# Performance work log

Hardware: AMD Instinct MI355X
Metric: run time of the kernel (lower is better)

Reference implementation:

```python
import jax, jax.numpy as jnp
import numpy as np

N_NODES = 50000
N_EDGES = 800000

def _gcn_layer(x, W, b, src, dst, n):
    # DGL GraphConv, norm='both': out = D_in^{-1/2} A D_out^{-1/2} x W + b
    e = src.shape[0]
    ones = jnp.ones((e,), dtype=x.dtype)
    deg_out = jax.ops.segment_sum(ones, src, num_segments=n)
    deg_in = jax.ops.segment_sum(ones, dst, num_segments=n)
    norm_src = jax.lax.rsqrt(jnp.clip(deg_out, 1.0))  # [n]
    norm_dst = jax.lax.rsqrt(jnp.clip(deg_in, 1.0))   # [n]
    # weight applied before aggregation (in_feats >= out_feats path in DGL)
    h = (x * norm_src[:, None]) @ W                   # [n, out]
    agg = jax.ops.segment_sum(h[src], dst, num_segments=n)  # SpMM: gather-scatter
    return agg * norm_dst[:, None] + b

def setup_inputs() -> dict:
    key = jax.random.key(0)
    ks = jax.random.split(key, 7)
    d_in, d_hid, d_out = 512, 256, 128
    features = jax.random.normal(ks[0], (N_NODES, d_in), dtype=jnp.float32)
    src = jax.random.randint(ks[1], (N_EDGES,), 0, N_NODES, dtype=jnp.int64)
    dst = jax.random.randint(ks[2], (N_EDGES,), 0, N_NODES, dtype=jnp.int64)
    W1 = jax.random.normal(ks[3], (d_in, d_hid), dtype=jnp.float32) / np.sqrt(d_in)
    b1 = jnp.zeros((d_hid,), dtype=jnp.float32)
    W2 = jax.random.normal(ks[4], (d_hid, d_out), dtype=jnp.float32) / np.sqrt(d_hid)
    b2 = jnp.zeros((d_out,), dtype=jnp.float32)
    return {"features": features, "src": src, "dst": dst,
            "W1": W1, "b1": b1, "W2": W2, "b2": b2}

def reference(features, src, dst, W1, b1, W2, b2):
    n = features.shape[0]
    x = _gcn_layer(features, W1, b1, src, dst, n)
    x = jax.nn.relu(x)
    x = _gcn_layer(x, W2, b2, src, dst, n)
    return x
```

## Files before the change

### kernel.cpp

```cpp
#include <hip/hip_runtime.h>
#include <type_traits>

#define DIN  512
#define DHID 256
#define DOF  128

#define RB   13
#define RSZ  (1 << RB)
#define BPR  32

typedef _Float16 f16;
typedef _Float16 f16x8 __attribute__((ext_vector_type(8)));
typedef _Float16 f16v4 __attribute__((ext_vector_type(4)));
typedef _Float16 f16v2 __attribute__((ext_vector_type(2)));
typedef float f32x4 __attribute__((ext_vector_type(4)));

__global__ __launch_bounds__(256) void hist_deg(const int* __restrict__ src,
                                                const int* __restrict__ dst, int e,
                                                int* __restrict__ cnt_out,
                                                int* __restrict__ cnt_in) {
    __shared__ int h_out[RSZ], h_in[RSZ];
    const int r = blockIdx.x / BPR, b = blockIdx.x % BPR;
    const int base = r << RB;
    const int tid = threadIdx.x;
    for (int j = tid; j < RSZ; j += 256) { h_out[j] = 0; h_in[j] = 0; }
    __syncthreads();

    const int ce = (((e + BPR - 1) / BPR) + 3) & ~3;
    const int s0 = b * ce, s1 = min(s0 + ce, e);
    for (int i = s0 + tid * 4; i < s1; i += 1024) {
        if (i + 3 < s1) {
            int4 sv = *(const int4*)(src + i);
            int4 dv = *(const int4*)(dst + i);
            int v;
            v = sv.x - base; if ((unsigned)v < RSZ) atomicAdd(&h_out[v], 1);
            v = sv.y - base; if ((unsigned)v < RSZ) atomicAdd(&h_out[v], 1);
            v = sv.z - base; if ((unsigned)v < RSZ) atomicAdd(&h_out[v], 1);
            v = sv.w - base; if ((unsigned)v < RSZ) atomicAdd(&h_out[v], 1);
            v = dv.x - base; if ((unsigned)v < RSZ) atomicAdd(&h_in[v], 1);
            v = dv.y - base; if ((unsigned)v < RSZ) atomicAdd(&h_in[v], 1);
            v = dv.z - base; if ((unsigned)v < RSZ) atomicAdd(&h_in[v], 1);
            v = dv.w - base; if ((unsigned)v < RSZ) atomicAdd(&h_in[v], 1);
        } else {
            for (int q = i; q < s1; ++q) {
                int v = src[q] - base; if ((unsigned)v < RSZ) atomicAdd(&h_out[v], 1);
                v = dst[q] - base;     if ((unsigned)v < RSZ) atomicAdd(&h_in[v], 1);
            }
        }
    }
    __syncthreads();
    int* co = cnt_out + (size_t)(r * BPR + b) * RSZ;
    int* ci = cnt_in  + (size_t)(r * BPR + b) * RSZ;
    for (int j = tid; j < RSZ; j += 256) { co[j] = h_out[j]; ci[j] = h_in[j]; }
}

__global__ void sum_base(const int* __restrict__ cnt_out, int* __restrict__ cnt_in,
                         int* __restrict__ deg_in,
                         float* __restrict__ norm_src, float* __restrict__ norm_dst, int n) {
    int d = blockIdx.x * blockDim.x + threadIdx.x;
    if (d >= n) return;
    const int r = d >> RB, j = d & (RSZ - 1);
    int* ci = cnt_in + (size_t)(r * BPR) * RSZ + j;
    int s = 0;
#pragma unroll 4
    for (int b = 0; b < BPR; ++b) {
        int c = ci[(size_t)b * RSZ];
        ci[(size_t)b * RSZ] = s;
        s += c;
    }
    deg_in[d] = s;
    norm_dst[d] = rsqrtf(fmaxf((float)s, 1.0f));
    const int* co = cnt_out + (size_t)(r * BPR) * RSZ + j;
    int s2 = 0;
#pragma unroll 4
    for (int b = 0; b < BPR; ++b) s2 += co[(size_t)b * RSZ];
    norm_src[d] = rsqrtf(fmaxf((float)s2, 1.0f));
}

__global__ __launch_bounds__(256) void scan_part(const int* __restrict__ deg,
                                                 int* __restrict__ partial, int n) {
    const int base = blockIdx.x * 1024;
    const int tid = threadIdx.x;
    int v = 0;
#pragma unroll
    for (int j = 0; j < 4; ++j) {
        int i = base + tid * 4 + j;
        if (i < n) v += deg[i];
    }
    for (int o = 1; o < 64; o <<= 1) v += __shfl_xor(v, o);
    __shared__ int wsum[4];
    if ((tid & 63) == 0) wsum[tid >> 6] = v;
    __syncthreads();
    if (tid == 0) partial[blockIdx.x] = wsum[0] + wsum[1] + wsum[2] + wsum[3];
}

__global__ __launch_bounds__(64) void scan_offsets(int* __restrict__ partial, int nb,
                                                   int* __restrict__ rowptr, int n) {
    const int l = threadIdx.x;
    int orig = (l < nb) ? partial[l] : 0;
    int v = orig;
    for (int o = 1; o < 64; o <<= 1) {
        int u = __shfl_up(v, o);
        if (l >= o) v += u;
    }
    if (l < nb) partial[l] = v - orig;
    if (l == nb - 1) rowptr[n] = v;
}

__global__ __launch_bounds__(256) void scan_apply(const int* __restrict__ deg,
                                                  const int* __restrict__ partial,
                                                  int* __restrict__ rowptr, int n) {
    const int base = blockIdx.x * 1024;
    const int tid = threadIdx.x;
    int x[4]; int s = 0;
#pragma unroll
    for (int j = 0; j < 4; ++j) {
        int i = base + tid * 4 + j;
        x[j] = (i < n) ? deg[i] : 0;
        s += x[j];
    }
    const int l = tid & 63, w = tid >> 6;
    int inc = s;
    for (int o = 1; o < 64; o <<= 1) {
        int u = __shfl_up(inc, o);
        if (l >= o) inc += u;
    }
    __shared__ int wsum[4];
    if (l == 63) wsum[w] = inc;
    __syncthreads();
    int wbase = 0;
    for (int q = 0; q < w; ++q) wbase += wsum[q];
    int excl = partial[blockIdx.x] + wbase + (inc - s);
#pragma unroll
    for (int j = 0; j < 4; ++j) {
        int i = base + tid * 4 + j;
        if (i < n) rowptr[i] = excl;
        excl += x[j];
    }
}

__global__ __launch_bounds__(256) void fill_csr2(const int* __restrict__ src,
                                                 const int* __restrict__ dst, int e,
                                                 const int* __restrict__ rowptr,
                                                 const int* __restrict__ base_in,
                                                 int* __restrict__ csr_src) {
    __shared__ int cur[RSZ];
    const int r = blockIdx.x / BPR, b = blockIdx.x % BPR;
    const int base = r << RB;
    const int tid = threadIdx.x;
    for (int j = tid; j < RSZ; j += 256) cur[j] = 0;
    __syncthreads();

    const int* bi = base_in + (size_t)(r * BPR + b) * RSZ;
    const int ce = (((e + BPR - 1) / BPR) + 3) & ~3;
    const int s0 = b * ce, s1 = min(s0 + ce, e);
    for (int i = s0 + tid * 4; i < s1; i += 1024) {
        if (i + 3 < s1) {
            int4 dv = *(const int4*)(dst + i);
            int4 sv = *(const int4*)(src + i);
            int v;
            v = dv.x - base; if ((unsigned)v < RSZ) { int p = atomicAdd(&cur[v], 1); csr_src[rowptr[base + v] + bi[v] + p] = sv.x; }
            v = dv.y - base; if ((unsigned)v < RSZ) { int p = atomicAdd(&cur[v], 1); csr_src[rowptr[base + v] + bi[v] + p] = sv.y; }
            v = dv.z - base; if ((unsigned)v < RSZ) { int p = atomicAdd(&cur[v], 1); csr_src[rowptr[base + v] + bi[v] + p] = sv.z; }
            v = dv.w - base; if ((unsigned)v < RSZ) { int p = atomicAdd(&cur[v], 1); csr_src[rowptr[base + v] + bi[v] + p] = sv.w; }
        } else {
            for (int q = i; q < s1; ++q) {
                int v = dst[q] - base;
                if ((unsigned)v < RSZ) { int p = atomicAdd(&cur[v], 1); csr_src[rowptr[base + v] + bi[v] + p] = src[q]; }
            }
        }
    }
}

__global__ void transpose_w(const float* __restrict__ W1, const float* __restrict__ W2,
                            f16* __restrict__ w1t, f16* __restrict__ w2t) {
    int t = blockIdx.x * blockDim.x + threadIdx.x;
    if (t < DIN * DHID) {
        int k = t / DHID, c = t % DHID;
        w1t[c * DIN + k] = (f16)W1[t];
    } else {
        int u = t - DIN * DHID;
        if (u < DHID * DOF) {
            int k = u / DOF, c = u % DOF;
            w2t[c * DHID + k] = (f16)W2[u];
        }
    }
}

template<int K, int N, bool A_F32>
__global__ __launch_bounds__(256) void mfma_gemm(const void* __restrict__ Aptr,
                                                 const float* __restrict__ norm,
                                                 const f16* __restrict__ Bt,
                                                 f16* __restrict__ H, int M) {
    constexpr int BM = 128, BN = 128, BK = 32;
    constexpr int NT = K / BK;
    __shared__ __align__(16) f16 smem[BM * BN];

    const int rbase = blockIdx.x * BM;
    const int nbj = blockIdx.y * BN;
    const int tid = threadIdx.x;
    const int l = tid & 63, wid = tid >> 6;
    const int wr = wid >> 1, wc = wid & 1;
    const int fr = l & 15, kg = l >> 4;

    int arow[2], achk[2];
    float ascale[2];
#pragma unroll
    for (int j = 0; j < 2; ++j) {
        int u = tid + j * 256;
        arow[j] = u >> 2; achk[j] = u & 3;
        if (A_F32) {
            int grow = rbase + arow[j];
            ascale[j] = (grow < M) ? norm[grow] : 0.0f;
        }
    }

    struct ABregs {
        float4 a0[2], a1[2];
        f16x8  a16[2];
        f16x8  b[2];
    };

    auto gload = [&](int k0) {
        ABregs r;
#pragma unroll
        for (int j = 0; j < 2; ++j) {
            int grow = rbase + arow[j];
            if (A_F32) {
                if (grow < M) {
                    const float* A = (const float*)Aptr + (long)grow * K + k0 + achk[j] * 8;
                    r.a0[j] = *(const float4*)A;
                    r.a1[j] = *(const float4*)(A + 4);
                } else {
                    r.a0[j] = make_float4(0.f, 0.f, 0.f, 0.f);
                    r.a1[j] = make_float4(0.f, 0.f, 0.f, 0.f);
                }
            } else {
                f16x8 v = {};
                if (grow < M)
                    v = *(const f16x8*)((const f16*)Aptr + (long)grow * K + k0 + achk[j] * 8);
                r.a16[j] = v;
            }
            r.b[j] = *(const f16x8*)(Bt + (long)(nbj + arow[j]) * K + k0 + achk[j] * 8);
        }
        return r;
    };

    auto swrite = [&](int buf, const ABregs& r) {
        f16* As = smem + buf * 8192;
        f16* Bs = As + 4096;
#pragma unroll
        for (int j = 0; j < 2; ++j) {
            f16x8 v;
            if (A_F32) {
                float s = ascale[j];
                v[0] = (f16)(r.a0[j].x * s); v[1] = (f16)(r.a0[j].y * s);
                v[2] = (f16)(r.a0[j].z * s); v[3] = (f16)(r.a0[j].w * s);
                v[4] = (f16)(r.a1[j].x * s); v[5] = (f16)(r.a1[j].y * s);
                v[6] = (f16)(r.a1[j].z * s); v[7] = (f16)(r.a1[j].w * s);
            } else {
                v = r.a16[j];
            }
            int ia = (arow[j] * BK + achk[j] * 8) ^ ((arow[j] & 7) << 3);
            *(f16x8*)&As[ia] = v;
            *(f16x8*)&Bs[ia] = r.b[j];
        }
    };

    f32x4 acc[4][4] = {};

    auto compute = [&](int buf) {
        const f16* As = smem + buf * 8192;
        const f16* Bs = As + 4096;
        f16x8 af[4], bf[4];
#pragma unroll
        for (int m = 0; m < 4; ++m) {
            int row = wr * 64 + m * 16 + fr;
            int ia = (row * BK + kg * 8) ^ ((row & 7) << 3);
            af[m] = *(const f16x8*)&As[ia];
        }
#pragma unroll
        for (int nf = 0; nf < 4; ++nf) {
            int c = wc * 64 + nf * 16 + fr;
            int ib = (c * BK + kg * 8) ^ ((c & 7) << 3);
            bf[nf] = *(const f16x8*)&Bs[ib];
        }
#pragma unroll
        for (int m = 0; m < 4; ++m)
#pragma unroll
            for (int nf = 0; nf < 4; ++nf)
                acc[m][nf] = __builtin_amdgcn_mfma_f32_16x16x32_f16(af[m], bf[nf], acc[m][nf], 0, 0, 0);
    };

    ABregs ra = gload(0);
    swrite(0, ra);
    ABregs rb = gload(BK);

#pragma unroll
    for (int kt = 0; kt < NT; kt += 2) {
        __syncthreads();
        if (kt + 2 < NT) ra = gload((kt + 2) * BK);
        compute(0);
        if (kt + 1 < NT) swrite(1, rb);
        if (kt + 1 < NT) {
            __syncthreads();
            if (kt + 3 < NT) rb = gload((kt + 3) * BK);
            compute(1);
            if (kt + 2 < NT) swrite(0, ra);
        }
    }

    __syncthreads();
#pragma unroll
    for (int m = 0; m < 4; ++m)
#pragma unroll
        for (int nf = 0; nf < 4; ++nf)
#pragma unroll
            for (int i = 0; i < 4; ++i) {
                int row = wr * 64 + m * 16 + (l >> 4) * 4 + i;
                int col = wc * 64 + nf * 16 + (l & 15);
                smem[row * BN + col] = (f16)acc[m][nf][i];
            }
    __syncthreads();
#pragma unroll
    for (int j = 0; j < 8; ++j) {
        int u = tid + j * 256;
        int row = u >> 4, cu = u & 15;
        int grow = rbase + row;
        if (grow < M)
            *(f16x8*)(H + (long)grow * N + nbj + cu * 8) =
                *(const f16x8*)&smem[row * BN + cu * 8];
    }
}

template<int F, bool RELU, bool FOLD, bool OUT_F16>
__global__ __launch_bounds__(256) void aggregate_wave(const f16* __restrict__ H,
                                                      const int* __restrict__ rowptr,
                                                      const int* __restrict__ csr_src,
                                                      const float* __restrict__ norm_dst,
                                                      const float* __restrict__ norm_src,
                                                      const float* __restrict__ bias,
                                                      void* __restrict__ outp, int n) {
    constexpr int VPL = F / 64;
    using vec = typename std::conditional<VPL == 4, f16v4, f16v2>::type;

    const int node = blockIdx.x * 4 + (threadIdx.x >> 6);
    if (node >= n) return;
    const int l = threadIdx.x & 63;
    const int c0 = l * VPL;
    const f16* __restrict__ Hc = H + c0;

    int k = rowptr[node];
    const int end = rowptr[node + 1];

    float acc[VPL] = {};
    for (; k + 3 < end; k += 4) {
        int s0 = csr_src[k];
        int s1 = csr_src[k + 1];
        int s2 = csr_src[k + 2];
        int s3 = csr_src[k + 3];
        vec v0 = *(const vec*)(Hc + (long)s0 * F);
        vec v1 = *(const vec*)(Hc + (long)s1 * F);
        vec v2 = *(const vec*)(Hc + (long)s2 * F);
        vec v3 = *(const vec*)(Hc + (long)s3 * F);
#pragma unroll
        for (int q = 0; q < VPL; ++q) acc[q] += (float)v0[q];
#pragma unroll
        for (int q = 0; q < VPL; ++q) acc[q] += (float)v1[q];
#pragma unroll
        for (int q = 0; q < VPL; ++q) acc[q] += (float)v2[q];
#pragma unroll
        for (int q = 0; q < VPL; ++q) acc[q] += (float)v3[q];
    }
    for (; k < end; ++k) {
        vec v = *(const vec*)(Hc + (long)csr_src[k] * F);
#pragma unroll
        for (int q = 0; q < VPL; ++q) acc[q] += (float)v[q];
    }

    const float nd = norm_dst[node];
    const float ns = FOLD ? norm_src[node] : 1.0f;
#pragma unroll
    for (int q = 0; q < VPL; ++q) {
        float v = acc[q] * nd + bias[c0 + q];
        if (RELU) v = fmaxf(v, 0.0f);
        acc[q] = v * ns;
    }

    if (OUT_F16) {
        vec o;
#pragma unroll
        for (int q = 0; q < VPL; ++q) o[q] = (f16)acc[q];
        *(vec*)((f16*)outp + (long)node * F + c0) = o;
    } else {
        float* op = (float*)outp + (long)node * F + c0;
        if (VPL == 2) {
            *(float2*)op = make_float2(acc[0], acc[1]);
        } else {
#pragma unroll
            for (int q = 0; q < VPL; ++q) op[q] = acc[q];
        }
    }
}

extern "C" void kernel_launch(void* const* d_in, const int* in_sizes, int n_in,
                              void* d_out, int out_size, void* d_ws, size_t ws_size,
                              hipStream_t stream) {
    const float* features = (const float*)d_in[0];
    const int*   src      = (const int*)d_in[1];
    const int*   dst      = (const int*)d_in[2];
    const float* W1       = (const float*)d_in[3];
    const float* b1       = (const float*)d_in[4];
    const float* W2       = (const float*)d_in[5];
    const float* b2       = (const float*)d_in[6];
    float* out = (float*)d_out;

    const int n = in_sizes[0] / DIN;
    const int e = in_sizes[1];

    const int ranges = (n + RSZ - 1) >> RB;
    const size_t cntsz = (size_t)ranges * BPR * RSZ;

    char* ws = (char*)d_ws;
    size_t off = 0;
    auto alloc = [&](size_t bytes) { size_t o = off; off += (bytes + 255) & ~(size_t)255; return o; };
    size_t o_degi   = alloc((size_t)n * 4);
    size_t o_nsrc   = alloc((size_t)n * 4);
    size_t o_ndst   = alloc((size_t)n * 4);
    size_t o_rowptr = alloc((size_t)(n + 1) * 4);
    size_t o_part   = alloc((size_t)64 * 4);
    size_t o_csr    = alloc((size_t)e * 4);
    size_t o_cnto   = alloc(cntsz * 4);
    size_t o_cnti   = alloc(cntsz * 4);
    size_t o_w1t    = alloc((size_t)DIN * DHID * 2);
    size_t o_w2t    = alloc((size_t)DHID * DOF * 2);
    size_t o_h1     = alloc((size_t)n * DHID * 2);
    size_t o_x1     = alloc((size_t)n * DHID * 2);
    size_t o_h2     = alloc((size_t)n * DOF * 2);
    (void)ws_size;

    int*   deg_in   = (int*)(ws + o_degi);
    float* norm_src = (float*)(ws + o_nsrc);
    float* norm_dst = (float*)(ws + o_ndst);
    int*   rowptr   = (int*)(ws + o_rowptr);
    int*   partial  = (int*)(ws + o_part);
    int*   csr_src  = (int*)(ws + o_csr);
    int*   cnt_out  = (int*)(ws + o_cnto);
    int*   cnt_in   = (int*)(ws + o_cnti);
    f16*   w1t      = (f16*)(ws + o_w1t);
    f16*   w2t      = (f16*)(ws + o_w2t);
    f16*   h1       = (f16*)(ws + o_h1);
    f16*   x1       = (f16*)(ws + o_x1);
    f16*   h2       = (f16*)(ws + o_h2);

    const int hblocks = ranges * BPR;
    hist_deg<<<hblocks, 256, 0, stream>>>(src, dst, e, cnt_out, cnt_in);
    sum_base<<<(n + 255) / 256, 256, 0, stream>>>(cnt_out, cnt_in, deg_in,
                                                  norm_src, norm_dst, n);
    const int nb = (n + 1023) / 1024;
    scan_part<<<nb, 256, 0, stream>>>(deg_in, partial, n);
    scan_offsets<<<1, 64, 0, stream>>>(partial, nb, rowptr, n);
    scan_apply<<<nb, 256, 0, stream>>>(deg_in, partial, rowptr, n);
    fill_csr2<<<hblocks, 256, 0, stream>>>(src, dst, e, rowptr, cnt_in, csr_src);
    transpose_w<<<(DIN * DHID + DHID * DOF + 255) / 256, 256, 0, stream>>>(W1, W2, w1t, w2t);

    const int mtiles = (n + 127) / 128;
    const int ablocks = (n + 3) / 4;

    mfma_gemm<DIN, DHID, true><<<dim3(mtiles, DHID / 128), 256, 0, stream>>>(
        features, norm_src, w1t, h1, n);
    aggregate_wave<DHID, true, true, true><<<ablocks, 256, 0, stream>>>(
        h1, rowptr, csr_src, norm_dst, norm_src, b1, x1, n);

    mfma_gemm<DHID, DOF, false><<<dim3(mtiles, DOF / 128), 256, 0, stream>>>(
        x1, nullptr, w2t, h2, n);
    aggregate_wave<DOF, false, false, false><<<ablocks, 256, 0, stream>>>(
        h2, rowptr, csr_src, norm_dst, norm_src, b2, out, n);
}
```

Before: 218.1 us.

## Use 16-byte gathers with multi-edge wave split in aggregation; deepen GEMM prefetch

The aggregation kernel now has each lane load 8 fp16 features (16 bytes) per gather, with the wave split into slots that each handle a different edge, followed by a cross-lane shuffle reduction. The goal is wider memory transactions and more edges in flight per wave for the gather-bound SpMM. The GEMM pipeline now keeps two K-tiles of global loads in registers, to hide more load latency. This costs extra registers, and the shuffle reduction adds overhead that may hurt when nodes have few edges.

```diff
diff --git a/kernel.cpp b/kernel.cpp
--- a/kernel.cpp
+++ b/kernel.cpp
@@ -11,8 +11,6 @@
 
 typedef _Float16 f16;
 typedef _Float16 f16x8 __attribute__((ext_vector_type(8)));
-typedef _Float16 f16v4 __attribute__((ext_vector_type(4)));
-typedef _Float16 f16v2 __attribute__((ext_vector_type(2)));
 typedef float f32x4 __attribute__((ext_vector_type(4)));
 
 __global__ __launch_bounds__(256) void hist_deg(const int* __restrict__ src,
@@ -292,21 +290,25 @@
                 acc[m][nf] = __builtin_amdgcn_mfma_f32_16x16x32_f16(af[m], bf[nf], acc[m][nf], 0, 0, 0);
     };
 
-    ABregs ra = gload(0);
-    swrite(0, ra);
-    ABregs rb = gload(BK);
+    ABregs rb, rc;
+    {
+        ABregs ra = gload(0);
+        swrite(0, ra);
+        rb = gload(BK);
+        if (NT > 2) rc = gload(2 * BK);
+    }
 
 #pragma unroll
     for (int kt = 0; kt < NT; kt += 2) {
         __syncthreads();
-        if (kt + 2 < NT) ra = gload((kt + 2) * BK);
         compute(0);
         if (kt + 1 < NT) swrite(1, rb);
+        if (kt + 3 < NT) rb = gload((kt + 3) * BK);
         if (kt + 1 < NT) {
             __syncthreads();
-            if (kt + 3 < NT) rb = gload((kt + 3) * BK);
             compute(1);
-            if (kt + 2 < NT) swrite(0, ra);
+            if (kt + 2 < NT) swrite(0, rc);
+            if (kt + 4 < NT) rc = gload((kt + 4) * BK);
         }
     }
 
@@ -334,71 +336,81 @@
 }
 
 template<int F, bool RELU, bool FOLD, bool OUT_F16>
-__global__ __launch_bounds__(256) void aggregate_wave(const f16* __restrict__ H,
-                                                      const int* __restrict__ rowptr,
-                                                      const int* __restrict__ csr_src,
-                                                      const float* __restrict__ norm_dst,
-                                                      const float* __restrict__ norm_src,
-                                                      const float* __restrict__ bias,
-                                                      void* __restrict__ outp, int n) {
-    constexpr int VPL = F / 64;
-    using vec = typename std::conditional<VPL == 4, f16v4, f16v2>::type;
+__global__ __launch_bounds__(256) void aggregate_vec(const f16* __restrict__ H,
+                                                     const int* __restrict__ rowptr,
+                                                     const int* __restrict__ csr_src,
+                                                     const float* __restrict__ norm_dst,
+                                                     const float* __restrict__ norm_src,
+                                                     const float* __restrict__ bias,
+                                                     void* __restrict__ outp, int n) {
+    constexpr int LR = F / 8;
+    constexpr int EPW = 64 / LR;
 
     const int node = blockIdx.x * 4 + (threadIdx.x >> 6);
     if (node >= n) return;
     const int l = threadIdx.x & 63;
-    const int c0 = l * VPL;
-    const f16* __restrict__ Hc = H + c0;
+    const int slot = l / LR;
+    const int col = (l & (LR - 1)) * 8;
+    const f16* __restrict__ Hc = H + col;
 
     int k = rowptr[node];
     const int end = rowptr[node + 1];
 
-    float acc[VPL] = {};
-    for (; k + 3 < end; k += 4) {
-        int s0 = csr_src[k];
-        int s1 = csr_src[k + 1];
-        int s2 = csr_src[k + 2];
-        int s3 = csr_src[k + 3];
-        vec v0 = *(const vec*)(Hc + (long)s0 * F);
-        vec v1 = *(const vec*)(Hc + (long)s1 * F);
-        vec v2 = *(const vec*)(Hc + (long)s2 * F);
-        vec v3 = *(const vec*)(Hc + (long)s3 * F);
-#pragma unroll
-        for (int q = 0; q < VPL; ++q) acc[q] += (float)v0[q];
-#pragma unroll
-        for (int q = 0; q < VPL; ++q) acc[q] += (float)v1[q];
-#pragma unroll
-        for (int q = 0; q < VPL; ++q) acc[q] += (float)v2[q];
-#pragma unroll
-        for (int q = 0; q < VPL; ++q) acc[q] += (float)v3[q];
-    }
-    for (; k < end; ++k) {
-        vec v = *(const vec*)(Hc + (long)csr_src[k] * F);
-#pragma unroll
-        for (int q = 0; q < VPL; ++q) acc[q] += (float)v[q];
+    float acc[8] = {};
+    for (; k + 4 * EPW <= end; k += 4 * EPW) {
+        int i0 = csr_src[k + slot];
+        int i1 = csr_src[k + EPW + slot];
+        int i2 = csr_src[k + 2 * EPW + slot];
+        int i3 = csr_src[k + 3 * EPW + slot];
+        f16x8 v0 = *(const f16x8*)(Hc + (long)i0 * F);
+        f16x8 v1 = *(const f16x8*)(Hc + (long)i1 * F);
+        f16x8 v2 = *(const f16x8*)(Hc + (long)i2 * F);
+        f16x8 v3 = *(const f16x8*)(Hc + (long)i3 * F);
+#pragma unroll
+        for (int q = 0; q < 8; ++q) acc[q] += (float)v0[q];
+#pragma unroll
+        for (int q = 0; q < 8; ++q) acc[q] += (float)v1[q];
+#pragma unroll
+        for (int q = 0; q < 8; ++q) acc[q] += (float)v2[q];
+#pragma unroll
+        for (int q = 0; q < 8; ++q) acc[q] += (float)v3[q];
+    }
+    for (; k < end; k += EPW) {
+        int idx = k + slot;
+        int ci = min(idx, end - 1);
+        int s = csr_src[ci];
+        f16x8 v = *(const f16x8*)(Hc + (long)s * F);
+        if (idx < end) {
+#pragma unroll
+            for (int q = 0; q < 8; ++q) acc[q] += (float)v[q];
+        }
+    }
+
+#pragma unroll
+    for (int o = LR; o < 64; o <<= 1) {
+#pragma unroll
+        for (int q = 0; q < 8; ++q) acc[q] += __shfl_xor(acc[q], o);
     }
 
     const float nd = norm_dst[node];
     const float ns = FOLD ? norm_src[node] : 1.0f;
 #pragma unroll
-    for (int q = 0; q < VPL; ++q) {
-        float v = acc[q] * nd + bias[c0 + q];
+    for (int q = 0; q < 8; ++q) {
+        float v = acc[q] * nd + bias[col + q];
         if (RELU) v = fmaxf(v, 0.0f);
         acc[q] = v * ns;
     }
 
-    if (OUT_F16) {
-        vec o;
-#pragma unroll
-        for (int q = 0; q < VPL; ++q) o[q] = (f16)acc[q];
-        *(vec*)((f16*)outp + (long)node * F + c0) = o;
-    } else {
-        float* op = (float*)outp + (long)node * F + c0;
-        if (VPL == 2) {
-            *(float2*)op = make_float2(acc[0], acc[1]);
+    if (slot == 0) {
+        if (OUT_F16) {
+            f16x8 o;
+#pragma unroll
+            for (int q = 0; q < 8; ++q) o[q] = (f16)acc[q];
+            *(f16x8*)((f16*)outp + (long)node * F + col) = o;
         } else {
-#pragma unroll
-            for (int q = 0; q < VPL; ++q) op[q] = acc[q];
+            float* op = (float*)outp + (long)node * F + col;
+            *(float4*)op = make_float4(acc[0], acc[1], acc[2], acc[3]);
+            *(float4*)(op + 4) = make_float4(acc[4], acc[5], acc[6], acc[7]);
         }
     }
 }
@@ -469,11 +481,11 @@
 
     mfma_gemm<DIN, DHID, true><<<dim3(mtiles, DHID / 128), 256, 0, stream>>>(
         features, norm_src, w1t, h1, n);
-    aggregate_wave<DHID, true, true, true><<<ablocks, 256, 0, stream>>>(
+    aggregate_vec<DHID, true, true, true><<<ablocks, 256, 0, stream>>>(
         h1, rowptr, csr_src, norm_dst, norm_src, b1, x1, n);
 
     mfma_gemm<DHID, DOF, false><<<dim3(mtiles, DOF / 128), 256, 0, stream>>>(
         x1, nullptr, w2t, h2, n);
-    aggregate_wave<DOF, false, false, false><<<ablocks, 256, 0, stream>>>(
+    aggregate_vec<DOF, false, false, false><<<ablocks, 256, 0, stream>>>(
         h2, rowptr, csr_src, norm_dst, norm_src, b2, out, n);
 }
```

New measurement: 210.9 us (median of 2 runs). 3.3% less time.
